# Kernel tuning notes

Measured on AMD Instinct MI355X. Metric: run time of the kernel, lower is better.

The kernel has to match this reference:

```python
import jax, jax.numpy as jnp
import numpy as np

N, E, F = 20000, 320000, 128
H = 2 * F  # MLP width = 256
EPS = 1e-5
TANH_ALPHA = 1.0


def setup_inputs() -> dict:
    key = jax.random.key(0)
    ks = jax.random.split(key, 16)
    x = jax.random.normal(ks[0], (N, F), dtype=jnp.float32)
    edge_index = jax.random.randint(ks[1], (2, E), 0, N, dtype=jnp.int64)
    s = 1.0 / np.sqrt(H)
    W1 = jax.random.uniform(ks[2], (H, H), jnp.float32, -s, s)
    b1 = jax.random.uniform(ks[3], (H,), jnp.float32, -s, s)
    g1 = jnp.ones((H,), jnp.float32)
    be1 = jnp.zeros((H,), jnp.float32)
    rm1 = jax.random.normal(ks[4], (H,), jnp.float32) * 0.1
    rv1 = jax.random.uniform(ks[5], (H,), jnp.float32, 0.5, 1.5)
    W2 = jax.random.uniform(ks[6], (H, H), jnp.float32, -s, s)
    b2 = jax.random.uniform(ks[7], (H,), jnp.float32, -s, s)
    g2 = jnp.ones((H,), jnp.float32)
    be2 = jnp.zeros((H,), jnp.float32)
    rm2 = jax.random.normal(ks[8], (H,), jnp.float32) * 0.1
    rv2 = jax.random.uniform(ks[9], (H,), jnp.float32, 0.5, 1.5)
    W3 = jax.random.uniform(ks[10], (F, H), jnp.float32, -s, s)
    b3 = jax.random.uniform(ks[11], (F,), jnp.float32, -s, s)
    return {"x": x, "edge_index": edge_index,
            "W1": W1, "b1": b1, "g1": g1, "be1": be1, "rm1": rm1, "rv1": rv1,
            "W2": W2, "b2": b2, "g2": g2, "be2": be2, "rm2": rm2, "rv2": rv2,
            "W3": W3, "b3": b3}


def _block(h, W, b, g, be, rm, rv):
    # Linear -> (Dropout inactive at eval) -> BatchNorm1d (eval, running stats) -> ReLU
    h = h @ W.T + b
    h = (h - rm) * (g * jax.lax.rsqrt(rv + EPS)) + be
    return jax.nn.relu(h)


def reference(x, edge_index, W1, b1, g1, be1, rm1, rv1,
              W2, b2, g2, be2, rm2, rv2, W3, b3):
    src, dst = edge_index[0], edge_index[1]  # PyG: x_j = x[src], x_i = x[dst]
    xi = x[dst]                              # [E, F]
    xj = x[src]                              # [E, F]
    h = jnp.concatenate([xi, xj - xi], axis=-1)  # [E, 2F]
    h = _block(h, W1, b1, g1, be1, rm1, rv1)
    h = _block(h, W2, b2, g2, be2, rm2, rv2)
    h = h @ W3.T + b3                        # [E, F]
    # scatter-mean aggregation over destination nodes
    summed = jax.ops.segment_sum(h, dst, num_segments=N)              # [N, F]
    cnt = jax.ops.segment_sum(jnp.ones((E,), h.dtype), dst, num_segments=N)
    agg = summed / jnp.maximum(cnt, 1.0)[:, None]
    return jnp.tanh(TANH_ALPHA * agg)
```

## Files before the change

### kernel.cpp

```cpp
#include <hip/hip_runtime.h>
#include <math.h>

#define NN 20000
#define EE 320000
#define FF 128
#define HH 256
#define MT 128

typedef _Float16 f16x8 __attribute__((ext_vector_type(8)));
typedef _Float16 f16x4 __attribute__((ext_vector_type(4)));
typedef float    f32x4 __attribute__((ext_vector_type(4)));

#define HADDR(m, bcol) (((m) << 9) + ((bcol) ^ (((m) & 7) << 4)))

#define WPTR_OFF  80000
#define SPAIR_OFF 160000
#define XH_OFF    1440000
#define W2F_OFF   6560000
#define W3F_OFF   6691072
#define WCF_OFF   6756608
#define PQ_OFF    6887680

#define PB_XH   2500
#define PB_HIST 1250
#define PB_W2   32
#define PB_WC   32
#define PB_W3   16
#define PREP_BLOCKS (PB_XH + PB_HIST + PB_W2 + PB_WC + PB_W3)

#define NODEB 313


__global__ __launch_bounds__(256) void prep_kernel(
    const float* __restrict__ x,  const int* __restrict__ eidx,
    const float* __restrict__ W1, const float* __restrict__ W2,
    const float* __restrict__ W3,
    _Float16* __restrict__ xh, _Float16* __restrict__ w2f,
    _Float16* __restrict__ wcf, _Float16* __restrict__ w3f,
    int* __restrict__ cnt)
{
    const int b = blockIdx.x, t = threadIdx.x;
    if (b < PB_XH) {
        const size_t base = ((size_t)b * 256 + t) * 4;
        float4 v = *(const float4*)(x + base);
        _Float16 o[4] = {(_Float16)v.x, (_Float16)v.y, (_Float16)v.z, (_Float16)v.w};
        __builtin_memcpy(xh + base, o, 8);
    } else if (b < PB_XH + PB_HIST) {
        const int e = (b - PB_XH) * 256 + t;
        atomicAdd(&cnt[eidx[EE + e]], 1);
    } else if (b < PB_XH + PB_HIST + PB_W2) {
        const int f = (b - (PB_XH + PB_HIST)) * 256 + t;
        const int n = ((f >> 9) << 4) | (f & 15);
        const int k = (((f >> 6) & 7) << 5) | (((f >> 4) & 3) << 3);
        const float* s = W2 + (size_t)n * HH + k;
        _Float16 o[8];
        #pragma unroll
        for (int j = 0; j < 8; ++j) o[j] = (_Float16)s[j];
        __builtin_memcpy(w2f + (size_t)f * 8, o, 16);
    } else if (b < PB_XH + PB_HIST + PB_W2 + PB_WC) {
        const int f = (b - (PB_XH + PB_HIST + PB_W2)) * 256 + t;
        const int n = ((f >> 8) << 4) | (f & 15);
        const int k = (((f >> 6) & 3) << 5) | (((f >> 4) & 3) << 3);
        _Float16 o[8];
        if (n < HH) {
            const float* a = W1 + (size_t)n * HH + k;
            #pragma unroll
            for (int j = 0; j < 8; ++j) o[j] = (_Float16)(a[j] - a[FF + j]);
        } else {
            const float* a = W1 + (size_t)(n - HH) * HH + FF + k;
            #pragma unroll
            for (int j = 0; j < 8; ++j) o[j] = (_Float16)a[j];
        }
        __builtin_memcpy(wcf + (size_t)f * 8, o, 16);
    } else {
        const int f = (b - (PB_XH + PB_HIST + PB_W2 + PB_WC)) * 256 + t;
        const int n = ((f >> 9) << 4) | (f & 15);
        const int k = (((f >> 6) & 7) << 5) | (((f >> 4) & 3) << 3);
        const float* s = W3 + (size_t)n * HH + k;
        _Float16 o[8];
        #pragma unroll
        for (int j = 0; j < 8; ++j) o[j] = (_Float16)s[j];
        __builtin_memcpy(w3f + (size_t)f * 8, o, 16);
    }
}

__global__ __launch_bounds__(512) void node_kernel(
    const _Float16* __restrict__ xh, const _Float16* __restrict__ wcf,
    const float* __restrict__ b1, const float* __restrict__ g1,
    const float* __restrict__ be1, const float* __restrict__ rm1,
    const float* __restrict__ rv1,
    _Float16* __restrict__ PQ,
    const int* __restrict__ cnt, int* __restrict__ wptr)
{
    if (blockIdx.x == NODEB) {
        __shared__ int sp[512];
        const int t = threadIdx.x;
        const int base = t * 40;
        int s = 0;
        #pragma unroll 1
        for (int i = 0; i < 40; ++i) { const int idx = base + i; if (idx < NN) s += cnt[idx]; }
        sp[t] = s;
        __syncthreads();
        for (int d = 1; d < 512; d <<= 1) {
            const int v = (t >= d) ? sp[t - d] : 0;
            __syncthreads();
            sp[t] += v;
            __syncthreads();
        }
        int run = sp[t] - s;
        #pragma unroll 1
        for (int i = 0; i < 40; ++i) {
            const int idx = base + i;
            if (idx < NN) { wptr[idx] = run; run += cnt[idx]; }
        }
        return;
    }

    const int tid = threadIdx.x;
    const int lane = tid & 63, wv = tid >> 6;
    const int lr = lane & 15, lq = lane >> 4;
    const int node0 = blockIdx.x * 64;

    f32x4 acc[4][4];
    #pragma unroll
    for (int i = 0; i < 4; ++i)
        #pragma unroll
        for (int j = 0; j < 4; ++j) acc[i][j] = (f32x4){0.f, 0.f, 0.f, 0.f};

    const f16x8* wb = (const f16x8*)wcf + (size_t)(wv * 16) * 64 + lane;
    #pragma unroll 1
    for (int kb = 0; kb < 4; ++kb) {
        f16x8 wf[4], af[4];
        #pragma unroll
        for (int j = 0; j < 4; ++j) wf[j] = wb[(j * 4 + kb) * 64];
        #pragma unroll
        for (int i = 0; i < 4; ++i) {
            int nd = node0 + i * 16 + lr;
            if (nd > NN - 1) nd = NN - 1;
            af[i] = *(const f16x8*)(xh + (size_t)nd * FF + kb * 32 + lq * 8);
        }
        #pragma unroll
        for (int i = 0; i < 4; ++i)
            #pragma unroll
            for (int j = 0; j < 4; ++j)
                acc[i][j] = __builtin_amdgcn_mfma_f32_16x16x32_f16(wf[j], af[i], acc[i][j], 0, 0, 0);
    }

    #pragma unroll
    for (int j = 0; j < 4; ++j) {
        const int n0 = wv * 64 + j * 16 + lq * 4;
        const int ch = (n0 < HH) ? n0 : n0 - HH;
        float sc[4], cc[4];
        #pragma unroll
        for (int r = 0; r < 4; ++r) {
            const float s1 = g1[ch + r] * rsqrtf(rv1[ch + r] + 1e-5f);
            sc[r] = s1;
            cc[r] = (n0 < HH) ? (b1[ch + r] - rm1[ch + r]) * s1 + be1[ch + r] : 0.f;
        }
        #pragma unroll
        for (int i = 0; i < 4; ++i) {
            const int nd = node0 + i * 16 + lr;
            if (nd < NN) {
                f16x4 o;
                #pragma unroll
                for (int r = 0; r < 4; ++r) o[r] = (_Float16)(acc[i][j][r] * sc[r] + cc[r]);
                *(f16x4*)(PQ + (size_t)nd * 512 + n0) = o;
            }
        }
    }
}

__global__ __launch_bounds__(256) void scatter_kernel(const int* __restrict__ eidx,
                                                      int* __restrict__ wptr,
                                                      unsigned int* __restrict__ spair)
{
    const int e = blockIdx.x * 256 + threadIdx.x;
    if (e < EE) {
        const int d = eidx[EE + e];
        const int pos = atomicAdd(&wptr[d], 1);
        spair[pos] = (unsigned int)eidx[e] | ((unsigned int)d << 16);
    }
}

__global__ __launch_bounds__(512, 4) void fused_edge_mlp(
    const _Float16* __restrict__ PQ,
    const unsigned int* __restrict__ spair,
    const _Float16* __restrict__ W2f,
    const float* __restrict__ b2, const float* __restrict__ g2,
    const float* __restrict__ be2, const float* __restrict__ rm2,
    const float* __restrict__ rv2,
    const _Float16* __restrict__ W3f,
    float* __restrict__ outp)
{
    __shared__ __align__(16) char shb[MT * 512];
    __shared__ __align__(16) float s_scale[HH];
    __shared__ __align__(16) float s_c[HH];
    __shared__ int s_dst[MT];

    const int tid = threadIdx.x;
    const int lane = tid & 63, wv = tid >> 6;
    const int lr = lane & 15, lq = lane >> 4;

    const int xcd = blockIdx.x & 7, bi = blockIdx.x >> 3;
    const int swz = (xcd < 4) ? (xcd * 313 + bi) : (1252 + (xcd - 4) * 312 + bi);
    const int e0 = swz * MT;

    {
        const int r = wv * 16 + lr;
        const int q = lq;
        const unsigned int pv = spair[e0 + r];
        const int dr = (int)(pv >> 16), sr = (int)(pv & 0xffffu);
        const f16x8* pd = (const f16x8*)(PQ + (size_t)dr * 512 + q * 64);
        const f16x8* ps = (const f16x8*)(PQ + (size_t)sr * 512 + 256 + q * 64);
        f16x8 av[8], bv[8];
        #pragma unroll
        for (int i = 0; i < 8; ++i) av[i] = pd[i];
        #pragma unroll
        for (int i = 0; i < 8; ++i) bv[i] = ps[i];

        if (tid < MT) s_dst[tid] = (int)(spair[e0 + tid] >> 16);
        if (tid < HH) {
            const float sc = g2[tid] * rsqrtf(rv2[tid] + 1e-5f);
            s_scale[tid] = sc;
            s_c[tid] = (b2[tid] - rm2[tid]) * sc + be2[tid];
        }

        #pragma unroll
        for (int i = 0; i < 8; ++i) {
            f16x8 s = av[i] + bv[i];
            f16x8 o;
            #pragma unroll
            for (int j = 0; j < 8; ++j) {
                const _Float16 z = (_Float16)0;
                o[j] = s[j] > z ? s[j] : z;
            }
            *(f16x8*)(shb + HADDR(r, q * 128 + i * 16)) = o;
        }
    }
    __syncthreads();

    {
        f32x4 acc[8][2];
        #pragma unroll
        for (int i = 0; i < 8; ++i) { acc[i][0] = (f32x4){0.f,0.f,0.f,0.f}; acc[i][1] = (f32x4){0.f,0.f,0.f,0.f}; }

        const int nt0 = wv * 2;
        const f16x8* wbase = (const f16x8*)W2f + lane;
        f16x8 cw0 = wbase[(nt0 * 8) * 64];
        f16x8 cw1 = wbase[((nt0 + 1) * 8) * 64];
        #pragma unroll 1
        for (int kb = 0; kb < 8; ++kb) {
            f16x8 nw0 = wbase[(nt0 * 8 + kb + 1) * 64];
            f16x8 nw1 = wbase[((nt0 + 1) * 8 + kb + 1) * 64];
            #pragma unroll
            for (int h = 0; h < 2; ++h) {
                f16x8 af[4];
                #pragma unroll
                for (int i = 0; i < 4; ++i) {
                    const int m = (h * 4 + i) * 16 + lr;
                    af[i] = *(const f16x8*)(shb + HADDR(m, kb * 64 + lq * 16));
                }
                #pragma unroll
                for (int i = 0; i < 4; ++i) {
                    acc[h*4+i][0] = __builtin_amdgcn_mfma_f32_16x16x32_f16(cw0, af[i], acc[h*4+i][0], 0, 0, 0);
                    acc[h*4+i][1] = __builtin_amdgcn_mfma_f32_16x16x32_f16(cw1, af[i], acc[h*4+i][1], 0, 0, 0);
                }
            }
            cw0 = nw0; cw1 = nw1;
        }
        __syncthreads();
        #pragma unroll
        for (int j = 0; j < 2; ++j) {
            const int n0 = (nt0 + j) * 16 + lq * 4;
            const float4 sc4 = *(const float4*)&s_scale[n0];
            const float4 cc4 = *(const float4*)&s_c[n0];
            #pragma unroll
            for (int i = 0; i < 8; ++i) {
                const int m = i * 16 + lr;
                f16x4 o;
                o[0] = (_Float16)fmaxf(acc[i][j][0] * sc4.x + cc4.x, 0.f);
                o[1] = (_Float16)fmaxf(acc[i][j][1] * sc4.y + cc4.y, 0.f);
                o[2] = (_Float16)fmaxf(acc[i][j][2] * sc4.z + cc4.z, 0.f);
                o[3] = (_Float16)fmaxf(acc[i][j][3] * sc4.w + cc4.w, 0.f);
                *(f16x4*)(shb + HADDR(m, n0 * 2)) = o;
            }
        }
        __syncthreads();
    }

    {
        f32x4 acc[8];
        #pragma unroll
        for (int i = 0; i < 8; ++i) acc[i] = (f32x4){0.f, 0.f, 0.f, 0.f};

        const int nt = wv;
        const f16x8* wbase = (const f16x8*)W3f + lane;
        f16x8 cw = wbase[(nt * 8) * 64];
        #pragma unroll 1
        for (int kb = 0; kb < 8; ++kb) {
            f16x8 nw = wbase[(nt * 8 + kb + 1) * 64];
            #pragma unroll
            for (int h = 0; h < 2; ++h) {
                f16x8 af[4];
                #pragma unroll
                for (int i = 0; i < 4; ++i) {
                    const int m = (h * 4 + i) * 16 + lr;
                    af[i] = *(const f16x8*)(shb + HADDR(m, kb * 64 + lq * 16));
                }
                #pragma unroll
                for (int i = 0; i < 4; ++i)
                    acc[h*4+i] = __builtin_amdgcn_mfma_f32_16x16x32_f16(cw, af[i], acc[h*4+i], 0, 0, 0);
            }
            cw = nw;
        }
        __syncthreads();
        const int n0 = nt * 16 + lq * 4;
        #pragma unroll
        for (int i = 0; i < 8; ++i)
            *(f32x4*)(shb + HADDR(i * 16 + lr, n0 * 4)) = acc[i];
        __syncthreads();

        {
            const int col = tid & 127;
            const int bc = col * 4;
            const int r0 = (tid >> 7) * 32;
            int cur = s_dst[r0];
            float run = 0.f;
            #pragma unroll 1
            for (int r = r0; r < r0 + 32; ++r) {
                const int d = s_dst[r];
                if (d != cur) {
                    atomicAdd(&outp[(size_t)cur * FF + col], run);
                    run = 0.f; cur = d;
                }
                run += *(const float*)(shb + HADDR(r, bc));
            }
            atomicAdd(&outp[(size_t)cur * FF + col], run);
        }
    }
}

__global__ __launch_bounds__(256) void finalize_kernel(const int* __restrict__ cnt,
                                                       const float* __restrict__ b3,
                                                       float* __restrict__ out)
{
    const int i4 = (blockIdx.x * 256 + threadIdx.x) * 4;
    if (i4 < NN * FF) {
        const float c = fmaxf((float)cnt[i4 >> 7], 1.0f);
        const float rc = 1.0f / c;
        float4 v = *(const float4*)(out + i4);
        const float* bb = b3 + (i4 & 127);
        v.x = tanhf(v.x * rc + bb[0]);
        v.y = tanhf(v.y * rc + bb[1]);
        v.z = tanhf(v.z * rc + bb[2]);
        v.w = tanhf(v.w * rc + bb[3]);
        *(float4*)(out + i4) = v;
    }
}

extern "C" void kernel_launch(void* const* d_in, const int* in_sizes, int n_in,
                              void* d_out, int out_size, void* d_ws, size_t ws_size,
                              hipStream_t stream)
{
    const float* x   = (const float*)d_in[0];
    const int*   ei  = (const int*)d_in[1];
    const float* W1  = (const float*)d_in[2];
    const float* b1  = (const float*)d_in[3];
    const float* g1  = (const float*)d_in[4];
    const float* be1 = (const float*)d_in[5];
    const float* rm1 = (const float*)d_in[6];
    const float* rv1 = (const float*)d_in[7];
    const float* W2  = (const float*)d_in[8];
    const float* b2  = (const float*)d_in[9];
    const float* g2  = (const float*)d_in[10];
    const float* be2 = (const float*)d_in[11];
    const float* rm2 = (const float*)d_in[12];
    const float* rv2 = (const float*)d_in[13];
    const float* W3  = (const float*)d_in[14];
    const float* b3  = (const float*)d_in[15];

    char* ws = (char*)d_ws;
    int* cnt_i = (int*)ws;
    int* wptr  = (int*)(ws + WPTR_OFF);
    unsigned int* spair = (unsigned int*)(ws + SPAIR_OFF);
    _Float16* xh  = (_Float16*)(ws + XH_OFF);
    _Float16* w2f = (_Float16*)(ws + W2F_OFF);
    _Float16* w3f = (_Float16*)(ws + W3F_OFF);
    _Float16* wcf = (_Float16*)(ws + WCF_OFF);
    _Float16* PQ  = (_Float16*)(ws + PQ_OFF);
    float* outp = (float*)d_out;

    hipMemsetAsync(cnt_i, 0, NN * sizeof(int), stream);
    hipMemsetAsync(d_out, 0, (size_t)NN * FF * sizeof(float), stream);

    prep_kernel<<<PREP_BLOCKS, 256, 0, stream>>>(x, ei, W1, W2, W3,
                                                 xh, w2f, wcf, w3f, cnt_i);
    node_kernel<<<NODEB + 1, 512, 0, stream>>>(xh, wcf, b1, g1, be1, rm1, rv1,
                                               PQ, cnt_i, wptr);
    scatter_kernel<<<(EE + 255) / 256, 256, 0, stream>>>(ei, wptr, spair);
    fused_edge_mlp<<<EE / MT, 512, 0, stream>>>(PQ, spair,
                                                w2f, b2, g2, be2, rm2, rv2,
                                                w3f, outp);
    finalize_kernel<<<(NN * FF / 4 + 255) / 256, 256, 0, stream>>>(cnt_i, b3, outp);
}
```

Baseline: 278.2 us.

## Switch edge MLP to 32x32 MFMA tiles and fold x conversion and output zeroing

```diff
diff --git a/kernel.cpp b/kernel.cpp
--- a/kernel.cpp
+++ b/kernel.cpp
@@ -9,56 +9,49 @@
 
 typedef _Float16 f16x8 __attribute__((ext_vector_type(8)));
 typedef _Float16 f16x4 __attribute__((ext_vector_type(4)));
-typedef float    f32x4 __attribute__((ext_vector_type(4)));
+typedef float    f32x4  __attribute__((ext_vector_type(4)));
+typedef float    f32x16 __attribute__((ext_vector_type(16)));
 
 #define HADDR(m, bcol) (((m) << 9) + ((bcol) ^ (((m) & 7) << 4)))
 
 #define WPTR_OFF  80000
 #define SPAIR_OFF 160000
-#define XH_OFF    1440000
 #define W2F_OFF   6560000
 #define W3F_OFF   6691072
 #define WCF_OFF   6756608
 #define PQ_OFF    6887680
 
-#define PB_XH   2500
 #define PB_HIST 1250
 #define PB_W2   32
 #define PB_WC   32
 #define PB_W3   16
-#define PREP_BLOCKS (PB_XH + PB_HIST + PB_W2 + PB_WC + PB_W3)
+#define PREP_BLOCKS (PB_HIST + PB_W2 + PB_WC + PB_W3)
 
 #define NODEB 313
 
 
 __global__ __launch_bounds__(256) void prep_kernel(
-    const float* __restrict__ x,  const int* __restrict__ eidx,
+    const int* __restrict__ eidx,
     const float* __restrict__ W1, const float* __restrict__ W2,
     const float* __restrict__ W3,
-    _Float16* __restrict__ xh, _Float16* __restrict__ w2f,
-    _Float16* __restrict__ wcf, _Float16* __restrict__ w3f,
-    int* __restrict__ cnt)
+    _Float16* __restrict__ w2f, _Float16* __restrict__ wcf,
+    _Float16* __restrict__ w3f, int* __restrict__ cnt)
 {
     const int b = blockIdx.x, t = threadIdx.x;
-    if (b < PB_XH) {
-        const size_t base = ((size_t)b * 256 + t) * 4;
-        float4 v = *(const float4*)(x + base);
-        _Float16 o[4] = {(_Float16)v.x, (_Float16)v.y, (_Float16)v.z, (_Float16)v.w};
-        __builtin_memcpy(xh + base, o, 8);
-    } else if (b < PB_XH + PB_HIST) {
-        const int e = (b - PB_XH) * 256 + t;
+    if (b < PB_HIST) {
+        const int e = b * 256 + t;
         atomicAdd(&cnt[eidx[EE + e]], 1);
-    } else if (b < PB_XH + PB_HIST + PB_W2) {
-        const int f = (b - (PB_XH + PB_HIST)) * 256 + t;
-        const int n = ((f >> 9) << 4) | (f & 15);
-        const int k = (((f >> 6) & 7) << 5) | (((f >> 4) & 3) << 3);
+    } else if (b < PB_HIST + PB_W2) {
+        const int f = (b - PB_HIST) * 256 + t;
+        const int n = ((f >> 10) << 5) | (f & 31);
+        const int k = (((f >> 6) & 15) << 4) | (((f >> 5) & 1) << 3);
         const float* s = W2 + (size_t)n * HH + k;
         _Float16 o[8];
         #pragma unroll
         for (int j = 0; j < 8; ++j) o[j] = (_Float16)s[j];
         __builtin_memcpy(w2f + (size_t)f * 8, o, 16);
-    } else if (b < PB_XH + PB_HIST + PB_W2 + PB_WC) {
-        const int f = (b - (PB_XH + PB_HIST + PB_W2)) * 256 + t;
+    } else if (b < PB_HIST + PB_W2 + PB_WC) {
+        const int f = (b - (PB_HIST + PB_W2)) * 256 + t;
         const int n = ((f >> 8) << 4) | (f & 15);
         const int k = (((f >> 6) & 3) << 5) | (((f >> 4) & 3) << 3);
         _Float16 o[8];
@@ -73,9 +66,9 @@
         }
         __builtin_memcpy(wcf + (size_t)f * 8, o, 16);
     } else {
-        const int f = (b - (PB_XH + PB_HIST + PB_W2 + PB_WC)) * 256 + t;
-        const int n = ((f >> 9) << 4) | (f & 15);
-        const int k = (((f >> 6) & 7) << 5) | (((f >> 4) & 3) << 3);
+        const int f = (b - (PB_HIST + PB_W2 + PB_WC)) * 256 + t;
+        const int n = ((f >> 10) << 5) | (f & 31);
+        const int k = (((f >> 6) & 15) << 4) | (((f >> 5) & 1) << 3);
         const float* s = W3 + (size_t)n * HH + k;
         _Float16 o[8];
         #pragma unroll
@@ -85,7 +78,7 @@
 }
 
 __global__ __launch_bounds__(512) void node_kernel(
-    const _Float16* __restrict__ xh, const _Float16* __restrict__ wcf,
+    const float* __restrict__ x, const _Float16* __restrict__ wcf,
     const float* __restrict__ b1, const float* __restrict__ g1,
     const float* __restrict__ be1, const float* __restrict__ rm1,
     const float* __restrict__ rv1,
@@ -98,7 +91,16 @@
         const int base = t * 40;
         int s = 0;
         #pragma unroll 1
-        for (int i = 0; i < 40; ++i) { const int idx = base + i; if (idx < NN) s += cnt[idx]; }
+        for (int g = 0; g < 5; ++g) {
+            int v[8];
+            #pragma unroll
+            for (int u = 0; u < 8; ++u) {
+                const int idx = base + g * 8 + u;
+                v[u] = (idx < NN) ? cnt[idx] : 0;
+            }
+            #pragma unroll
+            for (int u = 0; u < 8; ++u) s += v[u];
+        }
         sp[t] = s;
         __syncthreads();
         for (int d = 1; d < 512; d <<= 1) {
@@ -109,9 +111,18 @@
         }
         int run = sp[t] - s;
         #pragma unroll 1
-        for (int i = 0; i < 40; ++i) {
-            const int idx = base + i;
-            if (idx < NN) { wptr[idx] = run; run += cnt[idx]; }
+        for (int g = 0; g < 5; ++g) {
+            int v[8];
+            #pragma unroll
+            for (int u = 0; u < 8; ++u) {
+                const int idx = base + g * 8 + u;
+                v[u] = (idx < NN) ? cnt[idx] : 0;
+            }
+            #pragma unroll
+            for (int u = 0; u < 8; ++u) {
+                const int idx = base + g * 8 + u;
+                if (idx < NN) { wptr[idx] = run; run += v[u]; }
+            }
         }
         return;
     }
@@ -137,7 +148,15 @@
         for (int i = 0; i < 4; ++i) {
             int nd = node0 + i * 16 + lr;
             if (nd > NN - 1) nd = NN - 1;
-            af[i] = *(const f16x8*)(xh + (size_t)nd * FF + kb * 32 + lq * 8);
+            const float* xp = x + (size_t)nd * FF + kb * 32 + lq * 8;
+            const float4 xa = *(const float4*)xp;
+            const float4 xb = *(const float4*)(xp + 4);
+            f16x8 a;
+            a[0] = (_Float16)xa.x; a[1] = (_Float16)xa.y;
+            a[2] = (_Float16)xa.z; a[3] = (_Float16)xa.w;
+            a[4] = (_Float16)xb.x; a[5] = (_Float16)xb.y;
+            a[6] = (_Float16)xb.z; a[7] = (_Float16)xb.w;
+            af[i] = a;
         }
         #pragma unroll
         for (int i = 0; i < 4; ++i)
@@ -172,13 +191,18 @@
 
 __global__ __launch_bounds__(256) void scatter_kernel(const int* __restrict__ eidx,
                                                       int* __restrict__ wptr,
-                                                      unsigned int* __restrict__ spair)
-{
-    const int e = blockIdx.x * 256 + threadIdx.x;
-    if (e < EE) {
-        const int d = eidx[EE + e];
+                                                      unsigned int* __restrict__ spair,
+                                                      float* __restrict__ outp)
+{
+    const int idx = blockIdx.x * 256 + threadIdx.x;
+    float4* o4 = (float4*)outp;
+    #pragma unroll
+    for (int i = 0; i < 2; ++i)
+        o4[idx + i * 320000] = (float4){0.f, 0.f, 0.f, 0.f};
+    if (idx < EE) {
+        const int d = eidx[EE + idx];
         const int pos = atomicAdd(&wptr[d], 1);
-        spair[pos] = (unsigned int)eidx[e] | ((unsigned int)d << 16);
+        spair[pos] = (unsigned int)eidx[idx] | ((unsigned int)d << 16);
     }
 }
 
@@ -200,6 +224,7 @@
     const int tid = threadIdx.x;
     const int lane = tid & 63, wv = tid >> 6;
     const int lr = lane & 15, lq = lane >> 4;
+    const int l5 = lane & 31, hf = lane >> 5;
 
     const int xcd = blockIdx.x & 7, bi = blockIdx.x >> 3;
     const int swz = (xcd < 4) ? (xcd * 313 + bi) : (1252 + (xcd - 4) * 312 + bi);
@@ -240,100 +265,100 @@
     __syncthreads();
 
     {
-        f32x4 acc[8][2];
-        #pragma unroll
-        for (int i = 0; i < 8; ++i) { acc[i][0] = (f32x4){0.f,0.f,0.f,0.f}; acc[i][1] = (f32x4){0.f,0.f,0.f,0.f}; }
-
-        const int nt0 = wv * 2;
+        const int mt = wv & 3, nh = wv >> 2;
+        const int m = mt * 32 + l5;
+        f32x16 acc[4];
+        const f32x16 zz = {};
+        #pragma unroll
+        for (int j = 0; j < 4; ++j) acc[j] = zz;
+
         const f16x8* wbase = (const f16x8*)W2f + lane;
-        f16x8 cw0 = wbase[(nt0 * 8) * 64];
-        f16x8 cw1 = wbase[((nt0 + 1) * 8) * 64];
         #pragma unroll 1
-        for (int kb = 0; kb < 8; ++kb) {
-            f16x8 nw0 = wbase[(nt0 * 8 + kb + 1) * 64];
-            f16x8 nw1 = wbase[((nt0 + 1) * 8 + kb + 1) * 64];
-            #pragma unroll
-            for (int h = 0; h < 2; ++h) {
-                f16x8 af[4];
-                #pragma unroll
-                for (int i = 0; i < 4; ++i) {
-                    const int m = (h * 4 + i) * 16 + lr;
-                    af[i] = *(const f16x8*)(shb + HADDR(m, kb * 64 + lq * 16));
-                }
-                #pragma unroll
-                for (int i = 0; i < 4; ++i) {
-                    acc[h*4+i][0] = __builtin_amdgcn_mfma_f32_16x16x32_f16(cw0, af[i], acc[h*4+i][0], 0, 0, 0);
-                    acc[h*4+i][1] = __builtin_amdgcn_mfma_f32_16x16x32_f16(cw1, af[i], acc[h*4+i][1], 0, 0, 0);
-                }
-            }
-            cw0 = nw0; cw1 = nw1;
+        for (int ks = 0; ks < 16; ++ks) {
+            f16x8 wf[4];
+            #pragma unroll
+            for (int j = 0; j < 4; ++j)
+                wf[j] = wbase[((nh * 4 + j) * 16 + ks) * 64];
+            const f16x8 bf = *(const f16x8*)(shb + HADDR(m, ks * 32 + hf * 16));
+            #pragma unroll
+            for (int j = 0; j < 4; ++j)
+                acc[j] = __builtin_amdgcn_mfma_f32_32x32x16_f16(wf[j], bf, acc[j], 0, 0, 0);
         }
         __syncthreads();
         #pragma unroll
+        for (int j = 0; j < 4; ++j) {
+            const int ntile = nh * 4 + j;
+            #pragma unroll
+            for (int grp = 0; grp < 4; ++grp) {
+                const int n0 = ntile * 32 + grp * 8 + hf * 4;
+                const float4 sc4 = *(const float4*)&s_scale[n0];
+                const float4 cc4 = *(const float4*)&s_c[n0];
+                f16x4 o;
+                o[0] = (_Float16)fmaxf(acc[j][grp * 4 + 0] * sc4.x + cc4.x, 0.f);
+                o[1] = (_Float16)fmaxf(acc[j][grp * 4 + 1] * sc4.y + cc4.y, 0.f);
+                o[2] = (_Float16)fmaxf(acc[j][grp * 4 + 2] * sc4.z + cc4.z, 0.f);
+                o[3] = (_Float16)fmaxf(acc[j][grp * 4 + 3] * sc4.w + cc4.w, 0.f);
+                *(f16x4*)(shb + HADDR(m, n0 * 2)) = o;
+            }
+        }
+        __syncthreads();
+    }
+
+    {
+        const int mt = wv & 3, nh = wv >> 2;
+        const int m = mt * 32 + l5;
+        f32x16 acc[2];
+        const f32x16 zz = {};
+        acc[0] = zz; acc[1] = zz;
+
+        const f16x8* wbase = (const f16x8*)W3f + lane;
+        #pragma unroll 1
+        for (int ks = 0; ks < 16; ++ks) {
+            f16x8 wf[2];
+            #pragma unroll
+            for (int j = 0; j < 2; ++j)
+                wf[j] = wbase[((nh * 2 + j) * 16 + ks) * 64];
+            const f16x8 bf = *(const f16x8*)(shb + HADDR(m, ks * 32 + hf * 16));
+            #pragma unroll
+            for (int j = 0; j < 2; ++j)
+                acc[j] = __builtin_amdgcn_mfma_f32_32x32x16_f16(wf[j], bf, acc[j], 0, 0, 0);
+        }
+        __syncthreads();
+        #pragma unroll
         for (int j = 0; j < 2; ++j) {
-            const int n0 = (nt0 + j) * 16 + lq * 4;
-            const float4 sc4 = *(const float4*)&s_scale[n0];
-            const float4 cc4 = *(const float4*)&s_c[n0];
-            #pragma unroll
-            for (int i = 0; i < 8; ++i) {
-                const int m = i * 16 + lr;
-                f16x4 o;
-                o[0] = (_Float16)fmaxf(acc[i][j][0] * sc4.x + cc4.x, 0.f);
-                o[1] = (_Float16)fmaxf(acc[i][j][1] * sc4.y + cc4.y, 0.f);
-                o[2] = (_Float16)fmaxf(acc[i][j][2] * sc4.z + cc4.z, 0.f);
-                o[3] = (_Float16)fmaxf(acc[i][j][3] * sc4.w + cc4.w, 0.f);
-                *(f16x4*)(shb + HADDR(m, n0 * 2)) = o;
-            }
-        }
-        __syncthreads();
-    }
-
-    {
-        f32x4 acc[8];
-        #pragma unroll
-        for (int i = 0; i < 8; ++i) acc[i] = (f32x4){0.f, 0.f, 0.f, 0.f};
-
-        const int nt = wv;
-        const f16x8* wbase = (const f16x8*)W3f + lane;
-        f16x8 cw = wbase[(nt * 8) * 64];
-        #pragma unroll 1
-        for (int kb = 0; kb < 8; ++kb) {
-            f16x8 nw = wbase[(nt * 8 + kb + 1) * 64];
-            #pragma unroll
-            for (int h = 0; h < 2; ++h) {
-                f16x8 af[4];
-                #pragma unroll
-                for (int i = 0; i < 4; ++i) {
-                    const int m = (h * 4 + i) * 16 + lr;
-                    af[i] = *(const f16x8*)(shb + HADDR(m, kb * 64 + lq * 16));
-                }
-                #pragma unroll
-                for (int i = 0; i < 4; ++i)
-                    acc[h*4+i] = __builtin_amdgcn_mfma_f32_16x16x32_f16(cw, af[i], acc[h*4+i], 0, 0, 0);
-            }
-            cw = nw;
-        }
-        __syncthreads();
-        const int n0 = nt * 16 + lq * 4;
-        #pragma unroll
-        for (int i = 0; i < 8; ++i)
-            *(f32x4*)(shb + HADDR(i * 16 + lr, n0 * 4)) = acc[i];
+            const int ntile = nh * 2 + j;
+            #pragma unroll
+            for (int grp = 0; grp < 4; ++grp) {
+                const int n0 = ntile * 32 + grp * 8 + hf * 4;
+                f32x4 o = { acc[j][grp * 4 + 0], acc[j][grp * 4 + 1],
+                            acc[j][grp * 4 + 2], acc[j][grp * 4 + 3] };
+                *(f32x4*)(shb + HADDR(m, n0 * 4)) = o;
+            }
+        }
         __syncthreads();
 
         {
             const int col = tid & 127;
-            const int bc = col * 4;
-            const int r0 = (tid >> 7) * 32;
+            const int bc  = col * 4;
+            const int r0  = (tid >> 7) * 32;
             int cur = s_dst[r0];
             float run = 0.f;
             #pragma unroll 1
-            for (int r = r0; r < r0 + 32; ++r) {
-                const int d = s_dst[r];
-                if (d != cur) {
-                    atomicAdd(&outp[(size_t)cur * FF + col], run);
-                    run = 0.f; cur = d;
+            for (int g = 0; g < 4; ++g) {
+                float v[8];
+                #pragma unroll
+                for (int u = 0; u < 8; ++u)
+                    v[u] = *(const float*)(shb + HADDR(r0 + g * 8 + u, bc));
+                #pragma unroll
+                for (int u = 0; u < 8; ++u) {
+                    const int r = r0 + g * 8 + u;
+                    const int d = s_dst[r];
+                    if (d != cur) {
+                        atomicAdd(&outp[(size_t)cur * FF + col], run);
+                        run = 0.f; cur = d;
+                    }
+                    run += v[u];
                 }
-                run += *(const float*)(shb + HADDR(r, bc));
             }
             atomicAdd(&outp[(size_t)cur * FF + col], run);
         }
@@ -383,7 +408,6 @@
     int* cnt_i = (int*)ws;
     int* wptr  = (int*)(ws + WPTR_OFF);
     unsigned int* spair = (unsigned int*)(ws + SPAIR_OFF);
-    _Float16* xh  = (_Float16*)(ws + XH_OFF);
     _Float16* w2f = (_Float16*)(ws + W2F_OFF);
     _Float16* w3f = (_Float16*)(ws + W3F_OFF);
     _Float16* wcf = (_Float16*)(ws + WCF_OFF);
@@ -391,13 +415,12 @@
     float* outp = (float*)d_out;
 
     hipMemsetAsync(cnt_i, 0, NN * sizeof(int), stream);
-    hipMemsetAsync(d_out, 0, (size_t)NN * FF * sizeof(float), stream);
-
-    prep_kernel<<<PREP_BLOCKS, 256, 0, stream>>>(x, ei, W1, W2, W3,
-                                                 xh, w2f, wcf, w3f, cnt_i);
-    node_kernel<<<NODEB + 1, 512, 0, stream>>>(xh, wcf, b1, g1, be1, rm1, rv1,
+
+    prep_kernel<<<PREP_BLOCKS, 256, 0, stream>>>(ei, W1, W2, W3,
+                                                 w2f, wcf, w3f, cnt_i);
+    node_kernel<<<NODEB + 1, 512, 0, stream>>>(x, wcf, b1, g1, be1, rm1, rv1,
                                                PQ, cnt_i, wptr);
-    scatter_kernel<<<(EE + 255) / 256, 256, 0, stream>>>(ei, wptr, spair);
+    scatter_kernel<<<(EE + 255) / 256, 256, 0, stream>>>(ei, wptr, spair, outp);
     fused_edge_mlp<<<EE / MT, 512, 0, stream>>>(PQ, spair,
                                                 w2f, b2, g2, be2, rm2, rv2,
                                                 w3f, outp);
```

Result: slower. 304.6 us (+9.5%).
